# Performance work log

Hardware: AMD Instinct MI355X
Metric: run time of the kernel (lower is better)

## Reference

```python
import jax, jax.numpy as jnp
import numpy as np
from jax import lax


def _lin_weights(in_size, out_size):
    # torch F.interpolate(mode='bilinear', align_corners=False) source indices
    scale = in_size / out_size
    src = (jnp.arange(out_size, dtype=jnp.float32) + 0.5) * scale - 0.5
    src = jnp.maximum(src, 0.0)
    i0 = jnp.minimum(jnp.floor(src).astype(jnp.int32), in_size - 1)
    i1 = jnp.minimum(i0 + 1, in_size - 1)
    w = src - i0.astype(jnp.float32)
    return i0, i1, w


def bilinear_resize(x, out_h, out_w):
    # x: (..., H, W) -> (..., out_h, out_w), separable bilinear
    H, W = x.shape[-2], x.shape[-1]
    i0, i1, wh = _lin_weights(H, out_h)
    j0, j1, ww = _lin_weights(W, out_w)
    x = x[..., i0, :] * (1.0 - wh)[:, None] + x[..., i1, :] * wh[:, None]
    x = x[..., :, j0] * (1.0 - ww) + x[..., :, j1] * ww
    return x


def setup_inputs() -> dict:
    key = jax.random.key(0)
    ks = jax.random.split(key, 16)
    b, H, W = 16, 56, 56
    n = H * W
    dim, heads, dh, agent_num = 512, 8, 64, 49
    ID = heads * dh  # inner_dim == dim
    s = 0.02
    return {
        'x': jax.random.normal(ks[0], (b, n, dim), jnp.float32),
        'H': H, 'W': W,
        'q_w': s * jax.random.normal(ks[1], (dim, ID), jnp.float32),
        'q_b': s * jax.random.normal(ks[2], (ID,), jnp.float32),
        'kv_w': s * jax.random.normal(ks[3], (dim, 2 * ID), jnp.float32),
        'kv_b': s * jax.random.normal(ks[4], (2 * ID,), jnp.float32),
        'proj_w': s * jax.random.normal(ks[5], (ID, dim), jnp.float32),
        'proj_b': s * jax.random.normal(ks[6], (dim,), jnp.float32),
        'dwc_w': s * jax.random.normal(ks[7], (ID, 1, 3, 3), jnp.float32),
        'dwc_b': s * jax.random.normal(ks[8], (ID,), jnp.float32),
        'an_bias': s * jax.random.normal(ks[9], (heads, agent_num, 7, 7), jnp.float32),
        'na_bias': s * jax.random.normal(ks[10], (heads, agent_num, 7, 7), jnp.float32),
        'ah_bias': s * jax.random.normal(ks[11], (1, heads, agent_num, H, 1), jnp.float32),
        'aw_bias': s * jax.random.normal(ks[12], (1, heads, agent_num, 1, W), jnp.float32),
        'ha_bias': s * jax.random.normal(ks[13], (1, heads, H, 1, agent_num), jnp.float32),
        'wa_bias': s * jax.random.normal(ks[14], (1, heads, 1, W, agent_num), jnp.float32),
    }


def reference(x, H, W, q_w, q_b, kv_w, kv_b, proj_w, proj_b, dwc_w, dwc_b,
              an_bias, na_bias, ah_bias, aw_bias, ha_bias, wa_bias):
    b, n, c = x.shape
    heads, agent_num = an_bias.shape[0], an_bias.shape[1]
    ID = q_w.shape[1]
    dh = ID // heads
    scale = dh ** -0.5
    pool = int(round(agent_num ** 0.5))  # 7

    q = x @ q_w + q_b                      # (b, n, ID)
    kv = x @ kv_w + kv_b                   # (b, n, 2*ID)  (sr_ratio == 1)
    k, v = kv[..., :ID], kv[..., ID:]

    # adaptive avg pool of q on the (H, W) grid -> agent tokens (b, agent_num, ID)
    qi = q.reshape(b, pool, H // pool, pool, W // pool, ID)
    agent = qi.mean(axis=(2, 4)).reshape(b, agent_num, ID)

    qh = q.reshape(b, n, heads, dh).transpose(0, 2, 1, 3)          # (b,h,n,d)
    kh = k.reshape(b, n, heads, dh).transpose(0, 2, 1, 3)
    vh = v.reshape(b, n, heads, dh).transpose(0, 2, 1, 3)
    ah = agent.reshape(b, agent_num, heads, dh).transpose(0, 2, 1, 3)  # (b,h,a,d)

    # stage 1: agent tokens attend to k/v, with interpolated + factored position bias
    pb1 = bilinear_resize(an_bias, H, W).reshape(1, heads, agent_num, n)
    pb2 = (ah_bias + aw_bias).reshape(1, heads, agent_num, n)
    s1 = jnp.einsum('bhad,bhnd->bhan', ah * scale, kh) + pb1 + pb2
    agent_attn = jax.nn.softmax(s1, axis=-1)                        # (b,h,a,n)
    agent_v = jnp.einsum('bhan,bhnd->bhad', agent_attn, vh)         # (b,h,a,d)

    # stage 2: queries attend to agent tokens
    ab1 = bilinear_resize(na_bias, H, W).reshape(1, heads, agent_num, n).transpose(0, 1, 3, 2)
    ab2 = (ha_bias + wa_bias).reshape(1, heads, n, agent_num)
    s2 = jnp.einsum('bhnd,bhad->bhna', qh * scale, ah) + ab1 + ab2
    q_attn = jax.nn.softmax(s2, axis=-1)                            # (b,h,n,a)
    out = jnp.einsum('bhna,bhad->bhnd', q_attn, agent_v)
    out = out.transpose(0, 2, 1, 3).reshape(b, n, ID)

    # depthwise 3x3 conv over v as spatial residual
    v_img = v.reshape(b, H, W, ID).transpose(0, 3, 1, 2)            # (b,ID,H,W)
    dwc = lax.conv_general_dilated(v_img, dwc_w, (1, 1), 'SAME',
                                   feature_group_count=ID,
                                   dimension_numbers=('NCHW', 'OIHW', 'NCHW'))
    dwc = dwc + dwc_b[None, :, None, None]
    out = out + dwc.transpose(0, 2, 3, 1).reshape(b, n, ID)

    return out @ proj_w + proj_b
```

## Files before the change

### kernel.cpp

```cpp
#include <hip/hip_runtime.h>
#include <hip/hip_bf16.h>

#define DEV __device__ __forceinline__

typedef __attribute__((ext_vector_type(4))) float f32x4;
typedef __attribute__((ext_vector_type(8))) short bf8_t;
typedef __attribute__((ext_vector_type(4))) unsigned int u32x4;

static constexpr float QSCALE = 0.125f;

DEV float bflo(unsigned int w){ union{unsigned int i; float f;} x; x.i = w << 16; return x.f; }
DEV float bfhi(unsigned int w){ union{unsigned int i; float f;} x; x.i = w & 0xffff0000u; return x.f; }
DEV float bf2f(unsigned short u){ union{unsigned int i; float f;} x; x.i = ((unsigned int)u) << 16; return x.f; }
DEV unsigned short f2bf(float f){
  union{float f; unsigned int i;} x; x.f = f;
  unsigned int i = x.i;
  i += 0x7fffu + ((i >> 16) & 1u);
  return (unsigned short)(i >> 16);
}
DEV unsigned int pack2(float a, float b){ return (unsigned int)f2bf(a) | ((unsigned int)f2bf(b) << 16); }

DEV void mfma_acc(f32x4& c, const bf8_t& a, const bf8_t& b){
  asm volatile("v_mfma_f32_16x16x32_bf16 %0, %1, %2, %0" : "+v"(c) : "v"(a), "v"(b));
}

DEV void cp16(unsigned short* l, const unsigned short* g){
  __builtin_amdgcn_global_load_lds(
      (const __attribute__((address_space(1))) unsigned int*)(const void*)g,
      (__attribute__((address_space(3))) unsigned int*)(void*)l, 16, 0, 0);
}

DEV float wred_max(float v){
  #pragma unroll
  for (int m = 1; m < 64; m <<= 1) v = fmaxf(v, __shfl_xor(v, m));
  return v;
}
DEV float wred_sum(float v){
  #pragma unroll
  for (int m = 1; m < 64; m <<= 1) v += __shfl_xor(v, m);
  return v;
}

__global__ void k_prep(const float* __restrict__ qw, const float* __restrict__ kvw,
                       const float* __restrict__ pw, const float* __restrict__ qb,
                       const float* __restrict__ kvb,
                       unsigned short* __restrict__ wqkvt, unsigned short* __restrict__ wprojt,
                       float* __restrict__ qkvbias){
  const int i0 = blockIdx.x * blockDim.x + threadIdx.x;
  const int stride = gridDim.x * blockDim.x;
  for (int idx = i0; idx < 1536*512; idx += stride){
    int n = idx >> 9, k = idx & 511;
    float v = (n < 512) ? qw[k*512 + n] : kvw[k*1024 + (n - 512)];
    wqkvt[idx] = f2bf(v);
  }
  for (int idx = i0; idx < 512*512; idx += stride){
    int n = idx >> 9, k = idx & 511;
    wprojt[idx] = f2bf(pw[k*512 + n]);
  }
  for (int idx = i0; idx < 1536; idx += stride)
    qkvbias[idx] = (idx < 512) ? qb[idx] : kvb[idx - 512];
}

__global__ void k_cvt_x(const float* __restrict__ x, unsigned short* __restrict__ xb){
  const long total8 = (long)50176*512/8;
  for (long i = (long)blockIdx.x*blockDim.x + threadIdx.x; i < total8; i += (long)gridDim.x*blockDim.x){
    const float4* p = (const float4*)(x + i*8);
    float4 a = p[0], b = p[1];
    u32x4 o;
    o.x = pack2(a.x, a.y); o.y = pack2(a.z, a.w);
    o.z = pack2(b.x, b.y); o.w = pack2(b.z, b.w);
    *(u32x4*)(xb + i*8) = o;
  }
}

template<bool OUT_BF>
__global__ __launch_bounds__(256) void k_gemm(const unsigned short* __restrict__ A,
    const unsigned short* __restrict__ Bt, const float* __restrict__ bias,
    void* __restrict__ Cp, const int N, const int nxb){
  __shared__ unsigned short Al[128][32];
  __shared__ unsigned short Bl[128][32];
  const int tid = threadIdx.x, lane = tid & 63, w = tid >> 6;
  const int bid = blockIdx.x;
  const int cxd = bid & 7, kk = bid >> 3;
  const int yi = kk / nxb, xb = kk - yi*nxb;
  const int m0 = (cxd + 8*yi) * 128, n0 = xb * 128;
  const int wr = (w >> 1) * 64, wc = (w & 1) * 64;
  const int fr = lane & 15, kg = lane >> 4;
  const int srow = lane >> 2, sp = lane & 3;

  const unsigned short* gA0 = A  + (size_t)(m0 + w*32 + srow)*512 + sp*8;
  const unsigned short* gA1 = gA0 + (size_t)16*512;
  const unsigned short* gB0 = Bt + (size_t)(n0 + w*32 + srow)*512 + sp*8;
  const unsigned short* gB1 = gB0 + (size_t)16*512;
  unsigned short* lA0 = &Al[w*32][0];
  unsigned short* lA1 = &Al[w*32 + 16][0];
  unsigned short* lB0 = &Bl[w*32][0];
  unsigned short* lB1 = &Bl[w*32 + 16][0];

  f32x4 acc[4][4] = {};
  for (int kt = 0; kt < 16; ++kt){
    const int k0 = kt * 32;
    __syncthreads();
    cp16(lA0, gA0 + k0);
    cp16(lA1, gA1 + k0);
    cp16(lB0, gB0 + k0);
    cp16(lB1, gB1 + k0);
    __syncthreads();
    bf8_t af[4], bfm[4];
    #pragma unroll
    for (int i = 0; i < 4; ++i){
      af[i]  = *(const bf8_t*)&Al[wr + i*16 + fr][kg*8];
      bfm[i] = *(const bf8_t*)&Bl[wc + i*16 + fr][kg*8];
    }
    #pragma unroll
    for (int i = 0; i < 4; ++i)
      #pragma unroll
      for (int j = 0; j < 4; ++j)
        mfma_acc(acc[i][j], af[i], bfm[j]);
  }
  const int rb = (lane >> 4) * 4;
  #pragma unroll
  for (int j = 0; j < 4; ++j){
    const int col = n0 + wc + j*16 + fr;
    const float bs = bias[col];
    #pragma unroll
    for (int i = 0; i < 4; ++i){
      #pragma unroll
      for (int r = 0; r < 4; ++r){
        const int row = m0 + wr + i*16 + rb + r;
        float v = acc[i][j][r] + bs;
        if (OUT_BF) ((unsigned short*)Cp)[(size_t)row*N + col] = f2bf(v);
        else        ((float*)Cp)[(size_t)row*N + col] = v;
      }
    }
  }
}

__global__ void k_pool(const unsigned short* __restrict__ qkv, float* __restrict__ agent){
  const int b = blockIdx.x / 49, a = blockIdx.x % 49;
  const int p1 = a / 7, p2 = a % 7;
  for (int c = threadIdx.x; c < 512; c += 256){
    float s = 0.f;
    for (int r = 0; r < 8; ++r)
      for (int cc = 0; cc < 8; ++cc){
        int pix = (p1*8 + r)*56 + p2*8 + cc;
        s += bf2f(qkv[((size_t)b*3136 + pix)*1536 + c]);
      }
    agent[((size_t)b*49 + a)*512 + c] = s * (1.0f/64.0f);
  }
}

DEV void lin_w(int o, int& i0, int& i1, float& w){
  float src = (o + 0.5f)*0.125f - 0.5f;
  src = fmaxf(src, 0.f);
  int f = (int)floorf(src);
  i0 = min(f, 6); i1 = min(i0 + 1, 6); w = src - (float)i0;
}

__global__ void k_pb(const float* __restrict__ an, const float* __restrict__ ahb,
                     const float* __restrict__ awb, float* __restrict__ pbs){
  const int tot = 8*49*3136;
  for (int idx = blockIdx.x*blockDim.x + threadIdx.x; idx < tot; idx += gridDim.x*blockDim.x){
    int n = idx % 3136, ha = idx / 3136;
    int y = n / 56, x = n % 56;
    int iy0, iy1, ix0, ix1; float wy, wx;
    lin_w(y, iy0, iy1, wy); lin_w(x, ix0, ix1, wx);
    const float* t = an + (size_t)ha*49;
    float v0 = t[iy0*7+ix0]*(1.f-wy) + t[iy1*7+ix0]*wy;
    float v1 = t[iy0*7+ix1]*(1.f-wy) + t[iy1*7+ix1]*wy;
    float v = v0*(1.f-wx) + v1*wx;
    pbs[idx] = v + ahb[ha*56 + y] + awb[ha*56 + x];
  }
}

__global__ void k_ab(const float* __restrict__ na, const float* __restrict__ hab,
                     const float* __restrict__ wab, float* __restrict__ absumT){
  const int tot = 8*49*3136;
  for (int idx = blockIdx.x*blockDim.x + threadIdx.x; idx < tot; idx += gridDim.x*blockDim.x){
    int n = idx % 3136, ha = idx / 3136;
    int a = ha % 49, h = ha / 49;
    int y = n / 56, x = n % 56;
    int iy0, iy1, ix0, ix1; float wy, wx;
    lin_w(y, iy0, iy1, wy); lin_w(x, ix0, ix1, wx);
    const float* t = na + (size_t)ha*49;
    float v0 = t[iy0*7+ix0]*(1.f-wy) + t[iy1*7+ix0]*wy;
    float v1 = t[iy0*7+ix1]*(1.f-wy) + t[iy1*7+ix1]*wy;
    float v = v0*(1.f-wx) + v1*wx;
    absumT[idx] = v + hab[(h*56+y)*49 + a] + wab[(h*56+x)*49 + a];
  }
}

__global__ __launch_bounds__(256) void k_attn1(const unsigned short* __restrict__ qkv,
    const float* __restrict__ agent, const float* __restrict__ pbs,
    float* __restrict__ pacc, float* __restrict__ pml){
  const int bi = blockIdx.x;
  const int sp = bi % 7, h = (bi/7) & 7, b = bi / 56;
  const int tid = threadIdx.x, lane = tid & 63, w = tid >> 6;
  const int c = lane & 15, kg = lane >> 4;

  __shared__ unsigned short ag[64][72];
  __shared__ unsigned short Kl[64][72];
  __shared__ unsigned short Vt[64][72];
  __shared__ unsigned short Pl[4][16][72];

  for (int it = tid; it < 64*8; it += 256){
    int a = it >> 3, o = it & 7;
    u32x4 wv = {0,0,0,0};
    if (a < 49){
      const float* p = agent + ((size_t)b*49 + a)*512 + h*64 + o*8;
      f32x4 lo = *(const f32x4*)p, hi = *(const f32x4*)(p+4);
      wv.x = pack2(lo.x*QSCALE, lo.y*QSCALE);
      wv.y = pack2(lo.z*QSCALE, lo.w*QSCALE);
      wv.z = pack2(hi.x*QSCALE, hi.y*QSCALE);
      wv.w = pack2(hi.z*QSCALE, hi.w*QSCALE);
    }
    *(u32x4*)&ag[a][o*8] = wv;
  }
  __syncthreads();
  bf8_t agf[2];
  agf[0] = *(const bf8_t*)&ag[w*16 + c][kg*8];
  agf[1] = *(const bf8_t*)&ag[w*16 + c][kg*8 + 32];

  const int aw = w*16 + c;
  const int amin = aw < 49 ? aw : 48;
  const bool areal = aw < 49;
  const float* pbrow = pbs + ((size_t)(h*49 + amin))*3136 + sp*448;

  float m_ = -1e30f, l_ = 0.f;
  f32x4 acc[4] = {};

  for (int t = 0; t < 7; ++t){
    const int gn0 = sp*448 + t*64;
    f32x4 pb4[4];
    #pragma unroll
    for (int i = 0; i < 4; ++i)
      pb4[i] = *(const f32x4*)(pbrow + t*64 + 16*i + 4*kg);

    __syncthreads();
    #pragma unroll
    for (int ii = 0; ii < 2; ++ii){
      int it = tid + ii*256;
      int pix = it >> 3, o = it & 7;
      const unsigned short* kp = qkv + ((size_t)b*3136 + gn0 + pix)*1536 + 512 + h*64 + o*8;
      *(u32x4*)&Kl[pix][o*8] = *(const u32x4*)kp;
    }
    #pragma unroll
    for (int ii = 0; ii < 2; ++ii){
      int it = tid + ii*256;
      int pix = it & 63, o = it >> 6;
      const unsigned short* vp = qkv + ((size_t)b*3136 + gn0 + pix)*1536 + 1024 + h*64 + o*8;
      u32x4 vv = *(const u32x4*)vp;
      unsigned int vals[4] = {vv.x, vv.y, vv.z, vv.w};
      #pragma unroll
      for (int q = 0; q < 4; ++q){
        Vt[o*8 + 2*q][pix]     = (unsigned short)(vals[q] & 0xffffu);
        Vt[o*8 + 2*q + 1][pix] = (unsigned short)(vals[q] >> 16);
      }
    }
    __syncthreads();

    f32x4 sa[4] = {};
    #pragma unroll
    for (int i = 0; i < 4; ++i){
      bf8_t kf0 = *(const bf8_t*)&Kl[i*16 + c][kg*8];
      bf8_t kf1 = *(const bf8_t*)&Kl[i*16 + c][kg*8 + 32];
      mfma_acc(sa[i], kf0, agf[0]);
      mfma_acc(sa[i], kf1, agf[1]);
    }

    float s16[4][4]; float mx = -1e30f;
    #pragma unroll
    for (int i = 0; i < 4; ++i)
      #pragma unroll
      for (int r = 0; r < 4; ++r){
        float sv = areal ? (sa[i][r] + pb4[i][r]) : -1e30f;
        s16[i][r] = sv; mx = fmaxf(mx, sv);
      }
    mx = fmaxf(mx, __shfl_xor(mx, 16));
    mx = fmaxf(mx, __shfl_xor(mx, 32));
    float mn = fmaxf(m_, mx);
    float al = __expf(m_ - mn);
    float rs = 0.f;
    #pragma unroll
    for (int i = 0; i < 4; ++i)
      #pragma unroll
      for (int r = 0; r < 4; ++r){
        float p = __expf(s16[i][r] - mn);
        s16[i][r] = p; rs += p;
      }
    rs += __shfl_xor(rs, 16);
    rs += __shfl_xor(rs, 32);
    m_ = mn; l_ = l_*al + rs;

    #pragma unroll
    for (int i = 0; i < 4; ++i){
      uint2 pw;
      pw.x = pack2(s16[i][0], s16[i][1]);
      pw.y = pack2(s16[i][2], s16[i][3]);
      *(uint2*)&Pl[w][c][16*i + 4*kg] = pw;
    }

    float al_s[4];
    #pragma unroll
    for (int r = 0; r < 4; ++r) al_s[r] = __shfl(al, 4*kg + r);
    #pragma unroll
    for (int j = 0; j < 4; ++j)
      #pragma unroll
      for (int r = 0; r < 4; ++r) acc[j][r] *= al_s[r];

    bf8_t pf0 = *(const bf8_t*)&Pl[w][c][kg*8];
    bf8_t pf1 = *(const bf8_t*)&Pl[w][c][kg*8 + 32];
    #pragma unroll
    for (int j = 0; j < 4; ++j){
      bf8_t vf0 = *(const bf8_t*)&Vt[j*16 + c][kg*8];
      bf8_t vf1 = *(const bf8_t*)&Vt[j*16 + c][kg*8 + 32];
      mfma_acc(acc[j], pf0, vf0);
      mfma_acc(acc[j], pf1, vf1);
    }
  }

  const int base = ((b*8 + h)*7 + sp)*49;
  #pragma unroll
  for (int r = 0; r < 4; ++r){
    const int a = w*16 + 4*kg + r;
    if (a < 49){
      float* dst = pacc + (size_t)(base + a)*64 + c;
      #pragma unroll
      for (int j = 0; j < 4; ++j) dst[16*j] = acc[j][r];
    }
  }
  if (kg == 0 && areal){
    pml[(base + aw)*2]     = m_;
    pml[(base + aw)*2 + 1] = l_;
  }
}

__global__ void k_merge(const float* __restrict__ pacc, const float* __restrict__ pml,
                        float* __restrict__ agentv){
  const int gw = blockIdx.x*4 + (threadIdx.x >> 6);
  const int lane = threadIdx.x & 63;
  if (gw >= 16*8*49) return;
  const int a = gw % 49, bh = gw / 49;
  float ms[7], ls[7], M = -1e30f;
  #pragma unroll
  for (int s = 0; s < 7; ++s){
    int base = (bh*7 + s)*49 + a;
    ms[s] = pml[base*2]; ls[s] = pml[base*2 + 1];
    M = fmaxf(M, ms[s]);
  }
  float L = 0.f, o = 0.f;
  #pragma unroll
  for (int s = 0; s < 7; ++s){
    float e = __expf(ms[s] - M);
    L += ls[s]*e;
    o += pacc[(size_t)((bh*7 + s)*49 + a)*64 + lane]*e;
  }
  agentv[(size_t)(bh*49 + a)*64 + lane] = o / L;
}

__global__ __launch_bounds__(256) void k_attn2(const unsigned short* __restrict__ qkv,
    const float* __restrict__ agent, const float* __restrict__ agentv,
    const float* __restrict__ absumT, unsigned short* __restrict__ outb){
  const int blk = blockIdx.x;
  const int bh = blk / 13, tloc = blk % 13;
  const int b = bh >> 3, h = bh & 7;
  const int tid = threadIdx.x, lane = tid & 63, w = tid >> 6;
  const int c = lane & 15, kg = lane >> 4;

  __shared__ unsigned short ag[64][72];
  __shared__ unsigned short avT[64][72];
  __shared__ unsigned short Pl[4][16][72];

  for (int it = tid; it < 64*8; it += 256){
    int a = it >> 3, o = it & 7;
    u32x4 wv = {0,0,0,0};
    if (a < 49){
      const float* p = agent + ((size_t)b*49 + a)*512 + h*64 + o*8;
      f32x4 lo = *(const f32x4*)p, hi = *(const f32x4*)(p+4);
      wv.x = pack2(lo.x*QSCALE, lo.y*QSCALE);
      wv.y = pack2(lo.z*QSCALE, lo.w*QSCALE);
      wv.z = pack2(hi.x*QSCALE, hi.y*QSCALE);
      wv.w = pack2(hi.z*QSCALE, hi.w*QSCALE);
    }
    *(u32x4*)&ag[a][o*8] = wv;
  }
  for (int it = tid; it < 64*64; it += 256){
    int a = it >> 6, d = it & 63;
    avT[d][a] = (a < 49) ? f2bf(agentv[((size_t)bh*49 + a)*64 + d]) : (unsigned short)0;
  }
  __syncthreads();

  const int ti = tloc*4 + w;
  if (ti >= 49) return;
  const int pix0 = ti*64;

  bf8_t af[4][2];
  #pragma unroll
  for (int i = 0; i < 4; ++i){
    af[i][0] = *(const bf8_t*)&ag[i*16 + c][kg*8];
    af[i][1] = *(const bf8_t*)&ag[i*16 + c][kg*8 + 32];
  }

  for (int j = 0; j < 4; ++j){
    const int pix = pix0 + 16*j + c;
    const unsigned short* qp = qkv + ((size_t)b*3136 + pix)*1536 + h*64;
    bf8_t qf0 = *(const bf8_t*)(qp + kg*8);
    bf8_t qf1 = *(const bf8_t*)(qp + kg*8 + 32);
    f32x4 sa[4] = {};
    #pragma unroll
    for (int i = 0; i < 4; ++i){
      mfma_acc(sa[i], af[i][0], qf0);
      mfma_acc(sa[i], af[i][1], qf1);
    }
    float s16[4][4]; float mx = -1e30f;
    #pragma unroll
    for (int i = 0; i < 4; ++i){
      #pragma unroll
      for (int r = 0; r < 4; ++r){
        int a = 16*i + 4*kg + r;
        int am = a < 49 ? a : 48;
        float bias = absumT[((size_t)h*49 + am)*3136 + pix];
        float sv = (a < 49) ? (sa[i][r] + bias) : -1e30f;
        s16[i][r] = sv; mx = fmaxf(mx, sv);
      }
    }
    mx = fmaxf(mx, __shfl_xor(mx, 16));
    mx = fmaxf(mx, __shfl_xor(mx, 32));
    float rs = 0.f;
    #pragma unroll
    for (int i = 0; i < 4; ++i){
      #pragma unroll
      for (int r = 0; r < 4; ++r){
        float p = __expf(s16[i][r] - mx);
        s16[i][r] = p; rs += p;
      }
    }
    rs += __shfl_xor(rs, 16);
    rs += __shfl_xor(rs, 32);
    #pragma unroll
    for (int i = 0; i < 4; ++i){
      uint2 pw;
      pw.x = pack2(s16[i][0], s16[i][1]);
      pw.y = pack2(s16[i][2], s16[i][3]);
      *(uint2*)&Pl[w][c][16*i + 4*kg] = pw;
    }
    bf8_t pf0 = *(const bf8_t*)&Pl[w][c][kg*8];
    bf8_t pf1 = *(const bf8_t*)&Pl[w][c][kg*8 + 32];
    f32x4 acc[4] = {};
    #pragma unroll
    for (int jd = 0; jd < 4; ++jd){
      bf8_t vf0 = *(const bf8_t*)&avT[jd*16 + c][kg*8];
      bf8_t vf1 = *(const bf8_t*)&avT[jd*16 + c][kg*8 + 32];
      mfma_acc(acc[jd], pf0, vf0);
      mfma_acc(acc[jd], pf1, vf1);
    }
    float l_s[4];
    #pragma unroll
    for (int r = 0; r < 4; ++r) l_s[r] = __shfl(rs, 4*kg + r);
    #pragma unroll
    for (int r = 0; r < 4; ++r){
      const int prow = pix0 + 16*j + 4*kg + r;
      unsigned short* op = outb + ((size_t)b*3136 + prow)*512 + h*64;
      float inv = 1.0f / l_s[r];
      #pragma unroll
      for (int jd = 0; jd < 4; ++jd)
        op[jd*16 + c] = f2bf(acc[jd][r] * inv);
    }
  }
}

__global__ __launch_bounds__(256) void k_dwc(const unsigned short* __restrict__ qkv,
    const float* __restrict__ dwcw, const float* __restrict__ dwcb,
    unsigned short* __restrict__ outb){
  const int b = blockIdx.x / 56, y = blockIdx.x % 56;
  const int tid = threadIdx.x;
  const int cg = tid & 127, xh = tid >> 7;
  const int c0 = cg*4;
  float wv[9][4], bv[4];
  #pragma unroll
  for (int j = 0; j < 4; ++j){
    bv[j] = dwcb[c0 + j];
    #pragma unroll
    for (int t = 0; t < 9; ++t) wv[t][j] = dwcw[(c0 + j)*9 + t];
  }
  for (int xi = 0; xi < 28; ++xi){
    const int x = xh*28 + xi;
    float o[4] = {bv[0], bv[1], bv[2], bv[3]};
    #pragma unroll
    for (int ky = 0; ky < 3; ++ky){
      int ny = y + ky - 1;
      if (ny < 0 || ny >= 56) continue;
      #pragma unroll
      for (int kx = 0; kx < 3; ++kx){
        int nx = x + kx - 1;
        if (nx < 0 || nx >= 56) continue;
        const unsigned short* vp = qkv + ((size_t)b*3136 + ny*56 + nx)*1536 + 1024 + c0;
        unsigned int v01 = *(const unsigned int*)vp;
        unsigned int v23 = *((const unsigned int*)vp + 1);
        const int t = ky*3 + kx;
        o[0] += wv[t][0]*bflo(v01); o[1] += wv[t][1]*bfhi(v01);
        o[2] += wv[t][2]*bflo(v23); o[3] += wv[t][3]*bfhi(v23);
      }
    }
    unsigned short* op = outb + ((size_t)b*3136 + y*56 + x)*512 + c0;
    unsigned int a01 = *(unsigned int*)op;
    unsigned int a23 = *((unsigned int*)op + 1);
    o[0] += bflo(a01); o[1] += bfhi(a01);
    o[2] += bflo(a23); o[3] += bfhi(a23);
    *(unsigned int*)op       = pack2(o[0], o[1]);
    *((unsigned int*)op + 1) = pack2(o[2], o[3]);
  }
}

extern "C" void kernel_launch(void* const* d_in, const int* in_sizes, int n_in,
                              void* d_out, int out_size, void* d_ws, size_t ws_size,
                              hipStream_t stream){
  const float* x       = (const float*)d_in[0];
  const float* q_w     = (const float*)d_in[3];
  const float* q_b     = (const float*)d_in[4];
  const float* kv_w    = (const float*)d_in[5];
  const float* kv_b    = (const float*)d_in[6];
  const float* proj_w  = (const float*)d_in[7];
  const float* proj_b  = (const float*)d_in[8];
  const float* dwc_w   = (const float*)d_in[9];
  const float* dwc_b   = (const float*)d_in[10];
  const float* an_bias = (const float*)d_in[11];
  const float* na_bias = (const float*)d_in[12];
  const float* ah_bias = (const float*)d_in[13];
  const float* aw_bias = (const float*)d_in[14];
  const float* ha_bias = (const float*)d_in[15];
  const float* wa_bias = (const float*)d_in[16];

  char* ws = (char*)d_ws;
  size_t off = 0;
  auto alloc = [&](size_t bytes) -> void* {
    void* p = ws + off;
    off += (bytes + 255) & ~(size_t)255;
    return p;
  };
  unsigned short* xb     = (unsigned short*)alloc((size_t)50176*512*2);
  unsigned short* qkv    = (unsigned short*)alloc((size_t)50176*1536*2);
  unsigned short* wqkvt  = (unsigned short*)alloc((size_t)1536*512*2);
  unsigned short* wprojt = (unsigned short*)alloc((size_t)512*512*2);
  float* qkvb   = (float*)alloc((size_t)1536*4);
  float* agent  = (float*)alloc((size_t)16*49*512*4);
  float* agentv = (float*)alloc((size_t)16*8*49*64*4);
  float* pbs    = (float*)alloc((size_t)8*49*3136*4);
  float* absumT = (float*)alloc((size_t)8*49*3136*4);
  float* pacc   = (float*)alloc((size_t)16*8*8*49*64*4);
  float* pml    = (float*)alloc((size_t)16*8*8*49*2*4);
  unsigned short* outb = (unsigned short*)alloc((size_t)50176*512*2);
  if (off > ws_size) return;

  k_prep<<<512, 256, 0, stream>>>(q_w, kv_w, proj_w, q_b, kv_b, wqkvt, wprojt, qkvb);
  k_cvt_x<<<2048, 256, 0, stream>>>(x, xb);
  k_gemm<true><<<4704, 256, 0, stream>>>(xb, wqkvt, qkvb, qkv, 1536, 12);
  k_pool<<<784, 256, 0, stream>>>(qkv, agent);
  k_pb<<<1024, 256, 0, stream>>>(an_bias, ah_bias, aw_bias, pbs);
  k_ab<<<1024, 256, 0, stream>>>(na_bias, ha_bias, wa_bias, absumT);
  k_attn1<<<896, 256, 0, stream>>>(qkv, agent, pbs, pacc, pml);
  k_merge<<<1568, 256, 0, stream>>>(pacc, pml, agentv);
  k_attn2<<<1664, 256, 0, stream>>>(qkv, agent, agentv, absumT, outb);
  k_dwc<<<896, 256, 0, stream>>>(qkv, dwc_w, dwc_b, outb);
  k_gemm<false><<<1568, 256, 0, stream>>>(outb, wprojt, proj_b, d_out, 512, 4);
}
```

Measured before the change: 404.4 us.

## Double GEMM K-tile to 64 with XOR-swizzled LDS and fuse bias-table kernels

The bf16 GEMM now stages 64-wide K tiles instead of 32, which halves the number of barrier pairs per tile. It stores rows in LDS with an XOR swizzle on the 16-byte chunks to avoid bank conflicts on the fragment reads. The MFMA loop reuses each B fragment pair across four A fragments. Separately, the two positional-bias precompute kernels are merged into one launch that shares the interpolation index math. LDS use per block doubles, which may reduce occupancy.

```diff
diff --git a/kernel.cpp b/kernel.cpp
--- a/kernel.cpp
+++ b/kernel.cpp
@@ -77,8 +77,8 @@
 __global__ __launch_bounds__(256) void k_gemm(const unsigned short* __restrict__ A,
     const unsigned short* __restrict__ Bt, const float* __restrict__ bias,
     void* __restrict__ Cp, const int N, const int nxb){
-  __shared__ unsigned short Al[128][32];
-  __shared__ unsigned short Bl[128][32];
+  __shared__ unsigned short Al[128][64];
+  __shared__ unsigned short Bl[128][64];
   const int tid = threadIdx.x, lane = tid & 63, w = tid >> 6;
   const int bid = blockIdx.x;
   const int cxd = bid & 7, kk = bid >> 3;
@@ -86,39 +86,43 @@
   const int m0 = (cxd + 8*yi) * 128, n0 = xb * 128;
   const int wr = (w >> 1) * 64, wc = (w & 1) * 64;
   const int fr = lane & 15, kg = lane >> 4;
-  const int srow = lane >> 2, sp = lane & 3;
-
-  const unsigned short* gA0 = A  + (size_t)(m0 + w*32 + srow)*512 + sp*8;
-  const unsigned short* gA1 = gA0 + (size_t)16*512;
-  const unsigned short* gB0 = Bt + (size_t)(n0 + w*32 + srow)*512 + sp*8;
-  const unsigned short* gB1 = gB0 + (size_t)16*512;
-  unsigned short* lA0 = &Al[w*32][0];
-  unsigned short* lA1 = &Al[w*32 + 16][0];
-  unsigned short* lB0 = &Bl[w*32][0];
-  unsigned short* lB1 = &Bl[w*32 + 16][0];
+
+  const int lr = lane >> 3, slog = (lane & 7) ^ lr;
+  const unsigned short* gA = A  + (size_t)(m0 + w*32 + lr)*512 + slog*8;
+  const unsigned short* gB = Bt + (size_t)(n0 + w*32 + lr)*512 + slog*8;
 
   f32x4 acc[4][4] = {};
-  for (int kt = 0; kt < 16; ++kt){
-    const int k0 = kt * 32;
+  for (int kt = 0; kt < 8; ++kt){
+    const int k0 = kt * 64;
     __syncthreads();
-    cp16(lA0, gA0 + k0);
-    cp16(lA1, gA1 + k0);
-    cp16(lB0, gB0 + k0);
-    cp16(lB1, gB1 + k0);
+    #pragma unroll
+    for (int cch = 0; cch < 4; ++cch){
+      cp16(&Al[w*32 + cch*8][0], gA + (size_t)cch*8*512 + k0);
+      cp16(&Bl[w*32 + cch*8][0], gB + (size_t)cch*8*512 + k0);
+    }
     __syncthreads();
-    bf8_t af[4], bfm[4];
-    #pragma unroll
-    for (int i = 0; i < 4; ++i){
-      af[i]  = *(const bf8_t*)&Al[wr + i*16 + fr][kg*8];
-      bfm[i] = *(const bf8_t*)&Bl[wc + i*16 + fr][kg*8];
-    }
-    #pragma unroll
-    for (int i = 0; i < 4; ++i)
-      #pragma unroll
-      for (int j = 0; j < 4; ++j)
-        mfma_acc(acc[i][j], af[i], bfm[j]);
-  }
-  const int rb = (lane >> 4) * 4;
+    bf8_t afl[4], afh[4];
+    #pragma unroll
+    for (int i = 0; i < 4; ++i){
+      const int row = wr + i*16 + fr;
+      const int sl = (kg ^ (row & 7)) * 8;
+      afl[i] = *(const bf8_t*)&Al[row][sl];
+      afh[i] = *(const bf8_t*)&Al[row][sl ^ 32];
+    }
+    #pragma unroll
+    for (int j = 0; j < 4; ++j){
+      const int row = wc + j*16 + fr;
+      const int sl = (kg ^ (row & 7)) * 8;
+      bf8_t bfl = *(const bf8_t*)&Bl[row][sl];
+      bf8_t bfh = *(const bf8_t*)&Bl[row][sl ^ 32];
+      #pragma unroll
+      for (int i = 0; i < 4; ++i){
+        mfma_acc(acc[i][j], afl[i], bfl);
+        mfma_acc(acc[i][j], afh[i], bfh);
+      }
+    }
+  }
+  const int rb = kg * 4;
   #pragma unroll
   for (int j = 0; j < 4; ++j){
     const int col = n0 + wc + j*16 + fr;
@@ -157,24 +161,11 @@
   i0 = min(f, 6); i1 = min(i0 + 1, 6); w = src - (float)i0;
 }
 
-__global__ void k_pb(const float* __restrict__ an, const float* __restrict__ ahb,
-                     const float* __restrict__ awb, float* __restrict__ pbs){
-  const int tot = 8*49*3136;
-  for (int idx = blockIdx.x*blockDim.x + threadIdx.x; idx < tot; idx += gridDim.x*blockDim.x){
-    int n = idx % 3136, ha = idx / 3136;
-    int y = n / 56, x = n % 56;
-    int iy0, iy1, ix0, ix1; float wy, wx;
-    lin_w(y, iy0, iy1, wy); lin_w(x, ix0, ix1, wx);
-    const float* t = an + (size_t)ha*49;
-    float v0 = t[iy0*7+ix0]*(1.f-wy) + t[iy1*7+ix0]*wy;
-    float v1 = t[iy0*7+ix1]*(1.f-wy) + t[iy1*7+ix1]*wy;
-    float v = v0*(1.f-wx) + v1*wx;
-    pbs[idx] = v + ahb[ha*56 + y] + awb[ha*56 + x];
-  }
-}
-
-__global__ void k_ab(const float* __restrict__ na, const float* __restrict__ hab,
-                     const float* __restrict__ wab, float* __restrict__ absumT){
+__global__ void k_bias(const float* __restrict__ an, const float* __restrict__ ahb,
+                       const float* __restrict__ awb,
+                       const float* __restrict__ na, const float* __restrict__ hab,
+                       const float* __restrict__ wab,
+                       float* __restrict__ pbs, float* __restrict__ absumT){
   const int tot = 8*49*3136;
   for (int idx = blockIdx.x*blockDim.x + threadIdx.x; idx < tot; idx += gridDim.x*blockDim.x){
     int n = idx % 3136, ha = idx / 3136;
@@ -182,11 +173,20 @@
     int y = n / 56, x = n % 56;
     int iy0, iy1, ix0, ix1; float wy, wx;
     lin_w(y, iy0, iy1, wy); lin_w(x, ix0, ix1, wx);
-    const float* t = na + (size_t)ha*49;
-    float v0 = t[iy0*7+ix0]*(1.f-wy) + t[iy1*7+ix0]*wy;
-    float v1 = t[iy0*7+ix1]*(1.f-wy) + t[iy1*7+ix1]*wy;
-    float v = v0*(1.f-wx) + v1*wx;
-    absumT[idx] = v + hab[(h*56+y)*49 + a] + wab[(h*56+x)*49 + a];
+    {
+      const float* t = an + (size_t)ha*49;
+      float v0 = t[iy0*7+ix0]*(1.f-wy) + t[iy1*7+ix0]*wy;
+      float v1 = t[iy0*7+ix1]*(1.f-wy) + t[iy1*7+ix1]*wy;
+      float v = v0*(1.f-wx) + v1*wx;
+      pbs[idx] = v + ahb[ha*56 + y] + awb[ha*56 + x];
+    }
+    {
+      const float* t = na + (size_t)ha*49;
+      float v0 = t[iy0*7+ix0]*(1.f-wy) + t[iy1*7+ix0]*wy;
+      float v1 = t[iy0*7+ix1]*(1.f-wy) + t[iy1*7+ix1]*wy;
+      float v = v0*(1.f-wx) + v1*wx;
+      absumT[idx] = v + hab[(h*56+y)*49 + a] + wab[(h*56+x)*49 + a];
+    }
   }
 }
 
@@ -556,8 +556,7 @@
   k_cvt_x<<<2048, 256, 0, stream>>>(x, xb);
   k_gemm<true><<<4704, 256, 0, stream>>>(xb, wqkvt, qkvb, qkv, 1536, 12);
   k_pool<<<784, 256, 0, stream>>>(qkv, agent);
-  k_pb<<<1024, 256, 0, stream>>>(an_bias, ah_bias, aw_bias, pbs);
-  k_ab<<<1024, 256, 0, stream>>>(na_bias, ha_bias, wa_bias, absumT);
+  k_bias<<<1024, 256, 0, stream>>>(an_bias, ah_bias, aw_bias, na_bias, ha_bias, wa_bias, pbs, absumT);
   k_attn1<<<896, 256, 0, stream>>>(qkv, agent, pbs, pacc, pml);
   k_merge<<<1568, 256, 0, stream>>>(pacc, pml, agentv);
   k_attn2<<<1664, 256, 0, stream>>>(qkv, agent, agentv, absumT, outb);
```

New measurement: 381.1 us. 1.06x faster.
